# Performance work log

Measured on AMD Instinct MI355X. Metric: run time of the kernel, lower is better.

## Reference

```python
import jax, jax.numpy as jnp
import numpy as np

B, LQ, LK = 16, 256, 256
DQ = DK = DV = H = 256


def setup_inputs() -> dict:
    key = jax.random.key(0)
    ks = jax.random.split(key, 7)
    queries = jax.random.normal(ks[0], (B, LQ, DQ), dtype=jnp.float32)
    keys = jax.random.normal(ks[1], (B, LK, DK), dtype=jnp.float32)
    values = jax.random.normal(ks[2], (B, LK, DV), dtype=jnp.float32)
    valid_lens = jax.random.randint(ks[3], (B,), 1, LK + 1).astype(jnp.int32)
    W_q = jax.random.normal(ks[4], (DQ, H), dtype=jnp.float32) / np.sqrt(DQ)
    W_k = jax.random.normal(ks[5], (DK, H), dtype=jnp.float32) / np.sqrt(DK)
    w_v = jax.random.normal(ks[6], (H,), dtype=jnp.float32) / np.sqrt(H)
    return {"queries": queries, "keys": keys, "values": values,
            "valid_lens": valid_lens, "W_q": W_q, "W_k": W_k, "w_v": w_v}


def reference(queries, keys, values, valid_lens, W_q, W_k, w_v):
    # Project queries and keys to the hidden size (no bias)
    q = jnp.einsum('bqd,dh->bqh', queries, W_q)          # (B, Lq, H)
    k = jnp.einsum('bkd,dh->bkh', keys, W_k)             # (B, Lk, H)
    # Broadcast-add, tanh, then contract with w_v -> scores (B, Lq, Lk)
    features = jnp.tanh(q[:, :, None, :] + k[:, None, :, :])  # (B, Lq, Lk, H)
    scores = jnp.einsum('bqkh,h->bqk', features, w_v)
    # Masked softmax over last axis: positions >= valid_len get -1e6
    mask = jnp.arange(scores.shape[-1]) < valid_lens[:, None, None]  # (B,1,Lk) bcast
    scores = jnp.where(mask, scores, jnp.float32(-1e6))
    attn = jax.nn.softmax(scores, axis=-1)
    # Dropout is identity at inference (training=False)
    return jnp.einsum('bqk,bkv->bqv', attn, values)      # (B, Lq, Dv)
```

## Files before the change

kernel.cpp:

```cpp
#include <hip/hip_runtime.h>

using bf16x8 = __attribute__((ext_vector_type(8))) __bf16;
using f32x4  = __attribute__((ext_vector_type(4))) float;
using f32x2  = __attribute__((ext_vector_type(2))) float;
using us8    = __attribute__((ext_vector_type(8))) unsigned short;

#define TWO_LOG2E 2.8853900817779268f
#define LOG2E 1.4426950408889634f

__device__ __forceinline__ unsigned short f2bf(float x) {
  unsigned int u = __float_as_uint(x);
  u = (u + 0x7fffu + ((u >> 16) & 1u)) >> 16;
  return (unsigned short)u;
}
__device__ __forceinline__ float bf2f(unsigned short h) {
  return __uint_as_float(((unsigned int)h) << 16);
}
__device__ __forceinline__ f32x2 pk_fma(f32x2 a, f32x2 b, f32x2 c) {
  return __builtin_elementwise_fma(a, b, c);
}

__global__ __launch_bounds__(256) void tcast_kernel(
    const float* __restrict__ Wq, const float* __restrict__ Wk,
    const float* __restrict__ vals, const float* __restrict__ wv,
    unsigned short* __restrict__ wt_hi, unsigned short* __restrict__ wt_lo,
    unsigned short* __restrict__ vt_hi, unsigned short* __restrict__ vt_lo,
    float* __restrict__ wv2, float* __restrict__ Wsum) {
  if (blockIdx.x == 0) {
    int t = threadIdx.x;
    wv2[t] = -2.0f * wv[t];
    if (t < 64) {
      float s = wv[t] + wv[t + 64] + wv[t + 128] + wv[t + 192];
#pragma unroll
      for (int off = 1; off < 64; off <<= 1) s += __shfl_xor(s, off, 64);
      if (t == 0) Wsum[0] = s;
    }
  }
  __shared__ float tile[32][33];
  int m = blockIdx.x >> 6;
  int ts = blockIdx.x & 63;
  int R0 = (ts >> 3) << 5, C0 = (ts & 7) << 5;
  const float* src = (m == 0) ? Wq : (m == 1) ? Wk : (vals + ((m - 2) << 16));
  int r = threadIdx.x >> 3, c4 = (threadIdx.x & 7) << 2;
  float4 v = *(const float4*)(src + (R0 + r) * 256 + C0 + c4);
  tile[r][c4] = v.x; tile[r][c4 + 1] = v.y; tile[r][c4 + 2] = v.z; tile[r][c4 + 3] = v.w;
  __syncthreads();
  float o0 = tile[c4 + 0][r], o1 = tile[c4 + 1][r];
  float o2 = tile[c4 + 2][r], o3 = tile[c4 + 3][r];
  unsigned short h0 = f2bf(o0), h1 = f2bf(o1), h2 = f2bf(o2), h3 = f2bf(o3);
  int base = ((m < 2) ? (m << 16) : ((m - 2) << 16)) + (C0 + r) * 256 + R0 + c4;
  unsigned short* dh = (m < 2) ? wt_hi : vt_hi;
  unsigned short* dl = (m < 2) ? wt_lo : vt_lo;
  *(ushort4*)(dh + base) = make_ushort4(h0, h1, h2, h3);
  *(ushort4*)(dl + base) = make_ushort4(f2bf(o0 - bf2f(h0)), f2bf(o1 - bf2f(h1)),
                                        f2bf(o2 - bf2f(h2)), f2bf(o3 - bf2f(h3)));
}

__global__ __launch_bounds__(256, 4) void proj_kernel(
    const float* __restrict__ q, const float* __restrict__ kk,
    const unsigned short* __restrict__ w_hi, const unsigned short* __restrict__ w_lo,
    const int* __restrict__ vlens, float* __restrict__ Rq, float* __restrict__ RkT) {
  int wave = threadIdx.x >> 6, lane = threadIdx.x & 63;
  int mt = (blockIdx.x << 1) + (wave & 1);
  int m0 = mt << 4;
  int g = mt >> 8;
  if (g) {
    int bb = (m0 >> 8) & 15;
    if ((m0 & 255) >= vlens[bb]) return;
  }
  int r = lane & 15, qd = lane >> 4;
  int row = m0 + r;
  const float* A = (g == 0) ? (q + row * 256) : (kk + (row - 4096) * 256);
  int nbase = (blockIdx.y << 6) + ((wave >> 1) << 5);
  int boff0 = (g << 16) + (nbase + r) * 256 + qd * 8;
  int boff1 = boff0 + (16 << 8);
  f32x4 acc0 = {0.f, 0.f, 0.f, 0.f}, acc1 = {0.f, 0.f, 0.f, 0.f};
#pragma unroll
  for (int kh = 0; kh < 2; ++kh) {
    bf16x8 ah[4], al[4];
#pragma unroll
    for (int s = 0; s < 4; ++s) {
      const float* p = A + qd * 8 + (kh * 4 + s) * 32;
      float4 f0 = *(const float4*)p;
      float4 f1 = *(const float4*)(p + 4);
      float fv[8] = {f0.x, f0.y, f0.z, f0.w, f1.x, f1.y, f1.z, f1.w};
#pragma unroll
      for (int j = 0; j < 8; ++j) {
        __bf16 h = (__bf16)fv[j];
        ah[s][j] = h;
        al[s][j] = (__bf16)(fv[j] - (float)h);
      }
    }
#pragma unroll
    for (int s = 0; s < 4; ++s) {
      int off = (kh * 4 + s) * 32;
      bf16x8 bh0 = *(const bf16x8*)(w_hi + boff0 + off);
      bf16x8 bl0 = *(const bf16x8*)(w_lo + boff0 + off);
      acc0 = __builtin_amdgcn_mfma_f32_16x16x32_bf16(ah[s], bh0, acc0, 0, 0, 0);
      acc0 = __builtin_amdgcn_mfma_f32_16x16x32_bf16(ah[s], bl0, acc0, 0, 0, 0);
      acc0 = __builtin_amdgcn_mfma_f32_16x16x32_bf16(al[s], bh0, acc0, 0, 0, 0);
      bf16x8 bh1 = *(const bf16x8*)(w_hi + boff1 + off);
      bf16x8 bl1 = *(const bf16x8*)(w_lo + boff1 + off);
      acc1 = __builtin_amdgcn_mfma_f32_16x16x32_bf16(ah[s], bh1, acc1, 0, 0, 0);
      acc1 = __builtin_amdgcn_mfma_f32_16x16x32_bf16(ah[s], bl1, acc1, 0, 0, 0);
      acc1 = __builtin_amdgcn_mfma_f32_16x16x32_bf16(al[s], bh1, acc1, 0, 0, 0);
    }
  }
#pragma unroll
  for (int tI = 0; tI < 2; ++tI) {
    f32x4 acc = tI ? acc1 : acc0;
    int n0 = nbase + (tI << 4);
    f32x4 ex;
#pragma unroll
    for (int i = 0; i < 4; ++i) {
      float l = acc[i] * TWO_LOG2E;
      l = fminf(fmaxf(l, -27.f), 27.f);
      ex[i] = __builtin_amdgcn_exp2f(l);
    }
    if (g == 0) {
#pragma unroll
      for (int i = 0; i < 4; ++i)
        Rq[(m0 + qd * 4 + i) * 256 + n0 + r] = ex[i];
    } else {
      int b = (m0 >> 8) & 15;
      int kloc = (m0 & 255) + qd * 4;
      *(f32x4*)(RkT + (b << 16) + (n0 + r) * 256 + kloc) = ex;
    }
  }
}

__global__ __launch_bounds__(512) void sav_kernel(
    const float* __restrict__ Rq, const float* __restrict__ RkT,
    const float* __restrict__ wv2, const float* __restrict__ Wsum,
    const int* __restrict__ vlens,
    const unsigned short* __restrict__ vhi, const unsigned short* __restrict__ vlo,
    float* __restrict__ out) {
  __shared__ __align__(16) float rqs[16 * 260];
  __shared__ __align__(16) float kT[256 * 66];
  __shared__ __align__(16) float scs[16 * 264];
  unsigned short* athi = (unsigned short*)rqs;
  const int t = threadIdx.x;
  const int b = blockIdx.x;
  const int q0 = blockIdx.y << 4;
  const int qrow = (b << 8) + q0;
  const int vl = vlens[b];
  const int nkt64 = (vl + 63) >> 6;
  const int nkt   = (vl + 31) >> 5;
  const float wsum = Wsum[0];

  {
    int row = t >> 5, c0 = (t & 31) << 3;
    const float* g = Rq + (qrow + row) * 256 + c0;
    *(float4*)(rqs + row * 260 + c0)     = *(const float4*)g;
    *(float4*)(rqs + row * 260 + c0 + 4) = *(const float4*)(g + 4);
  }
  const int tq = t >> 5, tk = t & 31;
  const int hr = t >> 3, kc = (t & 7) << 3;

  for (int kt = 0; kt < nkt64; ++kt) {
    const int k0 = kt << 6;
    __syncthreads();
#pragma unroll
    for (int p = 0; p < 4; ++p) {
      int h = (p << 6) + hr;
      const float* gk = RkT + (b << 16) + h * 256 + k0 + kc;
      *(float4*)(kT + h * 66 + kc)     = *(const float4*)gk;
      *(float4*)(kT + h * 66 + kc + 4) = *(const float4*)(gk + 4);
    }
    __syncthreads();
    f32x2 a0 = {0.f, 0.f};
#pragma unroll 2
    for (int h = 0; h < 256; h += 4) {
      f32x4 qa = *(const f32x4*)(rqs + tq * 260 + h);
      f32x4 wm = *(const f32x4*)(wv2 + h);
#pragma unroll
      for (int j = 0; j < 4; ++j) {
        f32x2 rk = *(const f32x2*)(kT + (h + j) * 66 + (tk << 1));
        f32x2 d0 = pk_fma(rk, (f32x2)(qa[j]), (f32x2)(1.0f));
        f32x2 r0;
        r0.x = __uint_as_float(0x7EF311C3u - __float_as_uint(d0.x));
        r0.y = __uint_as_float(0x7EF311C3u - __float_as_uint(d0.y));
        r0 = r0 * pk_fma(-d0, r0, (f32x2)(2.0f));
        a0 = pk_fma(r0, (f32x2)(wm[j]), a0);
      }
    }
    a0 += (f32x2)(wsum);
    *(f32x2*)(scs + tq * 264 + k0 + (tk << 1)) = a0;
  }
  __syncthreads();

  {
    int row = t >> 5, c0 = (t & 31) << 3;
    const float* srow = scs + row * 264 + c0;
    float4 x0 = *(const float4*)(srow);
    float4 x1 = *(const float4*)(srow + 4);
    float p[8] = {x0.x, x0.y, x0.z, x0.w, x1.x, x1.y, x1.z, x1.w};
#pragma unroll
    for (int i = 0; i < 8; ++i)
      if (c0 + i >= vl) p[i] = -1e6f;
    float mx = p[0];
#pragma unroll
    for (int i = 1; i < 8; ++i) mx = fmaxf(mx, p[i]);
#pragma unroll
    for (int off = 1; off < 32; off <<= 1) mx = fmaxf(mx, __shfl_xor(mx, off, 64));
    float sm = 0.f;
#pragma unroll
    for (int i = 0; i < 8; ++i) {
      p[i] = __builtin_amdgcn_exp2f((p[i] - mx) * LOG2E);
      sm += p[i];
    }
#pragma unroll
    for (int off = 1; off < 32; off <<= 1) sm += __shfl_xor(sm, off, 64);
    float rs = __builtin_amdgcn_rcpf(sm);
    us8 vh;
#pragma unroll
    for (int i = 0; i < 8; ++i) vh[i] = f2bf(p[i] * rs);
    *(us8*)(athi + row * 264 + c0) = vh;
  }
  __syncthreads();

  {
    const int wave = t >> 6, lane = t & 63;
    const int r = lane & 15, qd = lane >> 4;
    const int nb = wave << 5;
    const int boff = (b << 16) + (nb + r) * 256 + qd * 8;
    f32x4 acc[2] = {{0.f,0.f,0.f,0.f},{0.f,0.f,0.f,0.f}};
    for (int s = 0; s < nkt; ++s) {
      bf16x8 pa = *(const bf16x8*)(athi + r * 264 + qd * 8 + s * 32);
#pragma unroll
      for (int tI = 0; tI < 2; ++tI) {
        bf16x8 bh = *(const bf16x8*)(vhi + boff + (tI << 12) + s * 32);
        bf16x8 bl = *(const bf16x8*)(vlo + boff + (tI << 12) + s * 32);
        acc[tI] = __builtin_amdgcn_mfma_f32_16x16x32_bf16(pa, bh, acc[tI], 0, 0, 0);
        acc[tI] = __builtin_amdgcn_mfma_f32_16x16x32_bf16(pa, bl, acc[tI], 0, 0, 0);
      }
    }
#pragma unroll
    for (int tI = 0; tI < 2; ++tI)
#pragma unroll
      for (int i = 0; i < 4; ++i)
        out[(b << 16) + (q0 + qd * 4 + i) * 256 + nb + (tI << 4) + r] = acc[tI][i];
  }
}

extern "C" void kernel_launch(void* const* d_in, const int* in_sizes, int n_in,
                              void* d_out, int out_size, void* d_ws, size_t ws_size,
                              hipStream_t stream) {
  const float* queries = (const float*)d_in[0];
  const float* keys    = (const float*)d_in[1];
  const float* values  = (const float*)d_in[2];
  const int*   vlens   = (const int*)d_in[3];
  const float* Wq      = (const float*)d_in[4];
  const float* Wk      = (const float*)d_in[5];
  const float* wv      = (const float*)d_in[6];
  float* out = (float*)d_out;
  char* ws = (char*)d_ws;

  unsigned short* wt_hi = (unsigned short*)(ws + 0);
  unsigned short* wt_lo = (unsigned short*)(ws + 262144);
  unsigned short* vt_hi = (unsigned short*)(ws + 524288);
  unsigned short* vt_lo = (unsigned short*)(ws + 2621440);
  float*          Rq    = (float*)(ws + 4718592);
  float*          RkT   = (float*)(ws + 8912896);
  float*          wv2   = (float*)(ws + 13107200);
  float*          Wsum  = (float*)(ws + 13108224);

  tcast_kernel<<<1152, 256, 0, stream>>>(Wq, Wk, values, wv,
                                         wt_hi, wt_lo, vt_hi, vt_lo, wv2, Wsum);
  proj_kernel<<<dim3(256, 4), 256, 0, stream>>>(queries, keys, wt_hi, wt_lo,
                                                vlens, Rq, RkT);
  sav_kernel<<<dim3(16, 16), 512, 0, stream>>>(Rq, RkT, wv2, Wsum, vlens,
                                               vt_hi, vt_lo, out);
}
```

Measured before the change: 145.7 us.

## Schedule score/softmax/AV work via persistent blocks pulling sorted jobs

The score kernel becomes persistent: 256 blocks repeatedly take 8-query jobs from an atomic counter, and the jobs are ordered by descending key-tile count so that batches with long valid lengths start first. The aim is to balance load across CUs when valid lengths vary per batch. The inner loop is also simplified from a packed Newton-refined reciprocal to one hardware rcp per element, with each wave handling one query row. Projection blocks now write zeros to the masked RkT tiles instead of returning early, which keeps the padded key entries well-defined. Costs are a single-thread job-list build, the atomic traffic, half-used MFMA tiles for the 8-row jobs, and possibly lower precision from the unrefined rcp.

```diff
diff --git a/kernel.cpp b/kernel.cpp
--- a/kernel.cpp
+++ b/kernel.cpp
@@ -16,16 +16,15 @@
 __device__ __forceinline__ float bf2f(unsigned short h) {
   return __uint_as_float(((unsigned int)h) << 16);
 }
-__device__ __forceinline__ f32x2 pk_fma(f32x2 a, f32x2 b, f32x2 c) {
-  return __builtin_elementwise_fma(a, b, c);
-}
 
 __global__ __launch_bounds__(256) void tcast_kernel(
     const float* __restrict__ Wq, const float* __restrict__ Wk,
     const float* __restrict__ vals, const float* __restrict__ wv,
+    const int* __restrict__ vlens,
     unsigned short* __restrict__ wt_hi, unsigned short* __restrict__ wt_lo,
     unsigned short* __restrict__ vt_hi, unsigned short* __restrict__ vt_lo,
-    float* __restrict__ wv2, float* __restrict__ Wsum) {
+    float* __restrict__ wv2, float* __restrict__ Wsum,
+    unsigned short* __restrict__ jobs, int* __restrict__ ctr) {
   if (blockIdx.x == 0) {
     int t = threadIdx.x;
     wv2[t] = -2.0f * wv[t];
@@ -34,6 +33,17 @@
 #pragma unroll
       for (int off = 1; off < 64; off <<= 1) s += __shfl_xor(s, off, 64);
       if (t == 0) Wsum[0] = s;
+    }
+    if (t == 0) {
+      ctr[0] = 0;
+      int n = 0;
+      for (int lvl = 4; lvl >= 1; --lvl)
+        for (int b = 0; b < 16; ++b) {
+          int kt = (vlens[b] + 63) >> 6;
+          if (kt == lvl)
+            for (int q = 0; q < 32; ++q)
+              jobs[n++] = (unsigned short)((b << 5) | q);
+        }
     }
   }
   __shared__ float tile[32][33];
@@ -64,14 +74,21 @@
   int mt = (blockIdx.x << 1) + (wave & 1);
   int m0 = mt << 4;
   int g = mt >> 8;
+  int r = lane & 15, qd = lane >> 4;
+  int nbase = (blockIdx.y << 6) + ((wave >> 1) << 5);
   if (g) {
     int bb = (m0 >> 8) & 15;
-    if ((m0 & 255) >= vlens[bb]) return;
-  }
-  int r = lane & 15, qd = lane >> 4;
+    if ((m0 & 255) >= vlens[bb]) {
+      f32x4 z = {0.f, 0.f, 0.f, 0.f};
+      int kloc = (m0 & 255) + qd * 4;
+#pragma unroll
+      for (int tI = 0; tI < 2; ++tI)
+        *(f32x4*)(RkT + (bb << 16) + (nbase + (tI << 4) + r) * 256 + kloc) = z;
+      return;
+    }
+  }
   int row = m0 + r;
   const float* A = (g == 0) ? (q + row * 256) : (kk + (row - 4096) * 256);
-  int nbase = (blockIdx.y << 6) + ((wave >> 1) << 5);
   int boff0 = (g << 16) + (nbase + r) * 256 + qd * 8;
   int boff1 = boff0 + (16 << 8);
   f32x4 acc0 = {0.f, 0.f, 0.f, 0.f}, acc1 = {0.f, 0.f, 0.f, 0.f};
@@ -129,117 +146,122 @@
   }
 }
 
-__global__ __launch_bounds__(512) void sav_kernel(
+__global__ __launch_bounds__(512) void sav3_kernel(
     const float* __restrict__ Rq, const float* __restrict__ RkT,
     const float* __restrict__ wv2, const float* __restrict__ Wsum,
-    const int* __restrict__ vlens,
+    const int* __restrict__ vlens, const unsigned short* __restrict__ jobs,
+    int* __restrict__ ctr,
     const unsigned short* __restrict__ vhi, const unsigned short* __restrict__ vlo,
     float* __restrict__ out) {
-  __shared__ __align__(16) float rqs[16 * 260];
-  __shared__ __align__(16) float kT[256 * 66];
-  __shared__ __align__(16) float scs[16 * 264];
-  unsigned short* athi = (unsigned short*)rqs;
+  __shared__ __align__(16) float kT[256 * 68];
+  __shared__ __align__(16) float rqs[8 * 260];
+  __shared__ __align__(16) float scs[8 * 260];
+  __shared__ __align__(16) unsigned short athi[16 * 264];
+  __shared__ float wv2s[256];
+  __shared__ int s_item;
   const int t = threadIdx.x;
-  const int b = blockIdx.x;
-  const int q0 = blockIdx.y << 4;
-  const int qrow = (b << 8) + q0;
-  const int vl = vlens[b];
-  const int nkt64 = (vl + 63) >> 6;
-  const int nkt   = (vl + 31) >> 5;
+  const int w = t >> 6, lane = t & 63;
   const float wsum = Wsum[0];
 
-  {
-    int row = t >> 5, c0 = (t & 31) << 3;
-    const float* g = Rq + (qrow + row) * 256 + c0;
-    *(float4*)(rqs + row * 260 + c0)     = *(const float4*)g;
-    *(float4*)(rqs + row * 260 + c0 + 4) = *(const float4*)(g + 4);
-  }
-  const int tq = t >> 5, tk = t & 31;
-  const int hr = t >> 3, kc = (t & 7) << 3;
-
-  for (int kt = 0; kt < nkt64; ++kt) {
-    const int k0 = kt << 6;
-    __syncthreads();
-#pragma unroll
-    for (int p = 0; p < 4; ++p) {
-      int h = (p << 6) + hr;
-      const float* gk = RkT + (b << 16) + h * 256 + k0 + kc;
-      *(float4*)(kT + h * 66 + kc)     = *(const float4*)gk;
-      *(float4*)(kT + h * 66 + kc + 4) = *(const float4*)(gk + 4);
-    }
-    __syncthreads();
-    f32x2 a0 = {0.f, 0.f};
-#pragma unroll 2
-    for (int h = 0; h < 256; h += 4) {
-      f32x4 qa = *(const f32x4*)(rqs + tq * 260 + h);
-      f32x4 wm = *(const f32x4*)(wv2 + h);
-#pragma unroll
-      for (int j = 0; j < 4; ++j) {
-        f32x2 rk = *(const f32x2*)(kT + (h + j) * 66 + (tk << 1));
-        f32x2 d0 = pk_fma(rk, (f32x2)(qa[j]), (f32x2)(1.0f));
-        f32x2 r0;
-        r0.x = __uint_as_float(0x7EF311C3u - __float_as_uint(d0.x));
-        r0.y = __uint_as_float(0x7EF311C3u - __float_as_uint(d0.y));
-        r0 = r0 * pk_fma(-d0, r0, (f32x2)(2.0f));
-        a0 = pk_fma(r0, (f32x2)(wm[j]), a0);
-      }
-    }
-    a0 += (f32x2)(wsum);
-    *(f32x2*)(scs + tq * 264 + k0 + (tk << 1)) = a0;
-  }
-  __syncthreads();
-
-  {
-    int row = t >> 5, c0 = (t & 31) << 3;
-    const float* srow = scs + row * 264 + c0;
-    float4 x0 = *(const float4*)(srow);
-    float4 x1 = *(const float4*)(srow + 4);
-    float p[8] = {x0.x, x0.y, x0.z, x0.w, x1.x, x1.y, x1.z, x1.w};
-#pragma unroll
-    for (int i = 0; i < 8; ++i)
-      if (c0 + i >= vl) p[i] = -1e6f;
-    float mx = p[0];
-#pragma unroll
-    for (int i = 1; i < 8; ++i) mx = fmaxf(mx, p[i]);
-#pragma unroll
-    for (int off = 1; off < 32; off <<= 1) mx = fmaxf(mx, __shfl_xor(mx, off, 64));
-    float sm = 0.f;
-#pragma unroll
-    for (int i = 0; i < 8; ++i) {
-      p[i] = __builtin_amdgcn_exp2f((p[i] - mx) * LOG2E);
-      sm += p[i];
-    }
-#pragma unroll
-    for (int off = 1; off < 32; off <<= 1) sm += __shfl_xor(sm, off, 64);
-    float rs = __builtin_amdgcn_rcpf(sm);
-    us8 vh;
-#pragma unroll
-    for (int i = 0; i < 8; ++i) vh[i] = f2bf(p[i] * rs);
-    *(us8*)(athi + row * 264 + c0) = vh;
-  }
-  __syncthreads();
-
-  {
-    const int wave = t >> 6, lane = t & 63;
-    const int r = lane & 15, qd = lane >> 4;
-    const int nb = wave << 5;
-    const int boff = (b << 16) + (nb + r) * 256 + qd * 8;
-    f32x4 acc[2] = {{0.f,0.f,0.f,0.f},{0.f,0.f,0.f,0.f}};
-    for (int s = 0; s < nkt; ++s) {
-      bf16x8 pa = *(const bf16x8*)(athi + r * 264 + qd * 8 + s * 32);
-#pragma unroll
-      for (int tI = 0; tI < 2; ++tI) {
-        bf16x8 bh = *(const bf16x8*)(vhi + boff + (tI << 12) + s * 32);
-        bf16x8 bl = *(const bf16x8*)(vlo + boff + (tI << 12) + s * 32);
-        acc[tI] = __builtin_amdgcn_mfma_f32_16x16x32_bf16(pa, bh, acc[tI], 0, 0, 0);
-        acc[tI] = __builtin_amdgcn_mfma_f32_16x16x32_bf16(pa, bl, acc[tI], 0, 0, 0);
-      }
-    }
-#pragma unroll
-    for (int tI = 0; tI < 2; ++tI)
+  if (t < 256) wv2s[t] = wv2[t];
+  for (int i = t; i < 8 * 264; i += 512) athi[8 * 264 + i] = 0;
+
+  for (;;) {
+    __syncthreads();
+    if (t == 0) s_item = atomicAdd(ctr, 1);
+    __syncthreads();
+    const int jid = s_item;
+    if (jid >= 512) return;
+    const int jw = jobs[jid];
+    const int b = jw >> 5, q0 = (jw & 31) << 3;
+    const int qrow = (b << 8) + q0;
+    const int vl = vlens[b];
+    const int ktiles = (vl + 63) >> 6;
+
+    {
+      int row = t >> 6, c = lane << 2;
+      *(float4*)(rqs + row * 260 + c) = *(const float4*)(Rq + (qrow + row) * 256 + c);
+    }
+    for (int kt = 0; kt < ktiles; ++kt) {
+      const int k0 = kt << 6;
+      __syncthreads();
+      {
+        int h0 = t >> 2, kc = (t & 3) << 4;
+#pragma unroll
+        for (int p = 0; p < 2; ++p) {
+          int h = h0 + (p << 7);
+          const float* gk = RkT + (b << 16) + h * 256 + k0 + kc;
+          *(float4*)(kT + h * 68 + kc)      = *(const float4*)gk;
+          *(float4*)(kT + h * 68 + kc + 4)  = *(const float4*)(gk + 4);
+          *(float4*)(kT + h * 68 + kc + 8)  = *(const float4*)(gk + 8);
+          *(float4*)(kT + h * 68 + kc + 12) = *(const float4*)(gk + 12);
+        }
+      }
+      __syncthreads();
+      float a = 0.f;
+#pragma unroll 4
+      for (int h = 0; h < 256; ++h) {
+        float qa = rqs[w * 260 + h];
+        float wm = wv2s[h];
+        float rk = kT[h * 68 + lane];
+        float d = __builtin_fmaf(rk, qa, 1.0f);
+        a = __builtin_fmaf(__builtin_amdgcn_rcpf(d), wm, a);
+      }
+      scs[w * 260 + k0 + lane] = a + wsum;
+    }
+    __syncthreads();
+
+    {
+      int c0 = lane << 2;
+      float4 x = *(const float4*)(scs + w * 260 + c0);
+      float p[4] = {x.x, x.y, x.z, x.w};
 #pragma unroll
       for (int i = 0; i < 4; ++i)
-        out[(b << 16) + (q0 + qd * 4 + i) * 256 + nb + (tI << 4) + r] = acc[tI][i];
+        if (c0 + i >= vl) p[i] = -1e6f;
+      float mx = fmaxf(fmaxf(p[0], p[1]), fmaxf(p[2], p[3]));
+#pragma unroll
+      for (int off = 1; off < 64; off <<= 1) mx = fmaxf(mx, __shfl_xor(mx, off, 64));
+      float sm = 0.f;
+#pragma unroll
+      for (int i = 0; i < 4; ++i) {
+        p[i] = __builtin_amdgcn_exp2f((p[i] - mx) * LOG2E);
+        sm += p[i];
+      }
+#pragma unroll
+      for (int off = 1; off < 64; off <<= 1) sm += __shfl_xor(sm, off, 64);
+      float rs = __builtin_amdgcn_rcpf(sm);
+      ushort4 vh;
+      vh.x = f2bf(p[0] * rs); vh.y = f2bf(p[1] * rs);
+      vh.z = f2bf(p[2] * rs); vh.w = f2bf(p[3] * rs);
+      *(ushort4*)(athi + w * 264 + c0) = vh;
+    }
+    __syncthreads();
+
+    {
+      const int r = lane & 15, qd = lane >> 4;
+      const int smax = (vl + 31) >> 5;
+      const int nb = w << 5;
+      const int boff = (b << 16) + (nb + r) * 256 + qd * 8;
+      f32x4 acc0 = {0.f, 0.f, 0.f, 0.f}, acc1 = {0.f, 0.f, 0.f, 0.f};
+      for (int s = 0; s < smax; ++s) {
+        bf16x8 pa = *(const bf16x8*)(athi + r * 264 + qd * 8 + s * 32);
+        bf16x8 bh0 = *(const bf16x8*)(vhi + boff + s * 32);
+        bf16x8 bl0 = *(const bf16x8*)(vlo + boff + s * 32);
+        acc0 = __builtin_amdgcn_mfma_f32_16x16x32_bf16(pa, bh0, acc0, 0, 0, 0);
+        acc0 = __builtin_amdgcn_mfma_f32_16x16x32_bf16(pa, bl0, acc0, 0, 0, 0);
+        bf16x8 bh1 = *(const bf16x8*)(vhi + boff + (16 << 8) + s * 32);
+        bf16x8 bl1 = *(const bf16x8*)(vlo + boff + (16 << 8) + s * 32);
+        acc1 = __builtin_amdgcn_mfma_f32_16x16x32_bf16(pa, bh1, acc1, 0, 0, 0);
+        acc1 = __builtin_amdgcn_mfma_f32_16x16x32_bf16(pa, bl1, acc1, 0, 0, 0);
+      }
+      if (qd < 2) {
+#pragma unroll
+        for (int i = 0; i < 4; ++i) {
+          out[(b << 16) + (q0 + qd * 4 + i) * 256 + nb + r]      = acc0[i];
+          out[(b << 16) + (q0 + qd * 4 + i) * 256 + nb + 16 + r] = acc1[i];
+        }
+      }
+    }
   }
 }
 
@@ -264,11 +286,14 @@
   float*          RkT   = (float*)(ws + 8912896);
   float*          wv2   = (float*)(ws + 13107200);
   float*          Wsum  = (float*)(ws + 13108224);
-
-  tcast_kernel<<<1152, 256, 0, stream>>>(Wq, Wk, values, wv,
-                                         wt_hi, wt_lo, vt_hi, vt_lo, wv2, Wsum);
+  unsigned short* jobs  = (unsigned short*)(ws + 13109248);
+  int*            ctr   = (int*)(ws + 13110272);
+
+  tcast_kernel<<<1152, 256, 0, stream>>>(Wq, Wk, values, wv, vlens,
+                                         wt_hi, wt_lo, vt_hi, vt_lo, wv2, Wsum,
+                                         jobs, ctr);
   proj_kernel<<<dim3(256, 4), 256, 0, stream>>>(queries, keys, wt_hi, wt_lo,
                                                 vlens, Rq, RkT);
-  sav_kernel<<<dim3(16, 16), 512, 0, stream>>>(Rq, RkT, wv2, Wsum, vlens,
-                                               vt_hi, vt_lo, out);
-}
+  sav3_kernel<<<256, 512, 0, stream>>>(Rq, RkT, wv2, Wsum, vlens, jobs, ctr,
+                                       vt_hi, vt_lo, out);
+}
```

Measured after the change: 146.0 us. About the same (+0.2%).
